# Performance work log

Hardware: AMD Instinct MI355X
Metric: run time of the kernel (lower is better)

## Reference

```python
import jax, jax.numpy as jnp
import numpy as np

N, T, D, H = 16, 1024, 1024, 1024


def setup_inputs() -> dict:
    key = jax.random.key(0)
    ks = jax.random.split(key, 7)
    x = jax.random.normal(ks[0], (N, T, D), dtype=jnp.float32)
    reset = jax.random.randint(ks[1], (N, T), 0, 2).astype(bool)
    carry = jax.random.normal(ks[2], (N, T, H), dtype=jnp.float32)
    # learned parameters (orthogonal-ish init approximated by scaled gaussian)
    initial_h = jax.random.normal(ks[3], (H,), dtype=jnp.float32) * 0.1
    w_i = jax.random.normal(ks[4], (D, 3 * H), dtype=jnp.float32) * (1.0 / np.sqrt(D))
    w_h = jax.random.normal(ks[5], (H, 3 * H), dtype=jnp.float32) * (1.0 / np.sqrt(H))
    b = jnp.zeros((3 * H,), dtype=jnp.float32)
    return {"x": x, "reset": reset, "carry": carry,
            "initial_h": initial_h, "w_i": w_i, "w_h": w_h, "b": b}


def _gru_scan(x, reset, carry, initial_h, w_i, w_h, b):
    n, t, _ = x.shape
    h_dim = initial_h.shape[0]
    # learn_initial_h and not is_target: replace carry with learned init where reset
    init_b = jnp.broadcast_to(initial_h, (n, t, h_dim))
    carry = jnp.where(reset[..., None], init_b, carry)
    # precompute input projections for all timesteps (math-equivalent hoist)
    gx = jnp.einsum('ntd,dk->ntk', x, w_i)  # [N,T,3H]
    w_h_zr, w_h_a = w_h[:, :2 * h_dim], w_h[:, 2 * h_dim:]
    b_zr, b_a = b[:2 * h_dim], b[2 * h_dim:]

    def step(h, inp):
        gx_t, reset_t, carry_t = inp  # [N,3H], [N], [N,H]
        h = jnp.where(reset_t[:, None], carry_t, h)
        zr = jax.nn.sigmoid(gx_t[:, :2 * h_dim] + h @ w_h_zr + b_zr)
        z, r = zr[:, :h_dim], zr[:, h_dim:]
        a = jnp.tanh(gx_t[:, 2 * h_dim:] + (r * h) @ w_h_a + b_a)
        h_next = (1.0 - z) * h + z * a
        return h_next, h_next

    h0 = carry[:, 0, :]  # scan init is carry_seq[:1,:] per batch element
    _, hs = jax.lax.scan(step, h0, (gx.transpose(1, 0, 2), reset.T, carry.transpose(1, 0, 2)))
    states = hs.transpose(1, 0, 2)  # [N,T,H]
    return states


def reference(x, reset, carry, initial_h, w_i, w_h, b):
    states = _gru_scan(x, reset, carry, initial_h, w_i, w_h, b)
    # hk.GRU returns (next_state, next_state): outputs_seq == states_seq
    return states, states, initial_h[None, :]
```

## Files before the change

### kernel.cpp

```cpp
#include <hip/hip_runtime.h>

typedef __attribute__((ext_vector_type(8))) short s8v;
typedef __attribute__((ext_vector_type(4))) float f4v;
typedef __attribute__((ext_vector_type(4))) unsigned int u4v;
typedef unsigned long long u64;

__device__ __forceinline__ float bf2f(unsigned short u) {
    union { float f; unsigned int i; } v; v.i = ((unsigned int)u) << 16; return v.f;
}
__device__ __forceinline__ unsigned short f2bf(float f) {
    union { float f; unsigned int i; } v; v.f = f;
    unsigned int x = v.i;
    return (unsigned short)((x + 0x7fffu + ((x >> 16) & 1u)) >> 16);
}
__device__ __forceinline__ float ldf(const void* p, size_t i, int f32) {
    return f32 ? ((const float*)p)[i] : bf2f(((const unsigned short*)p)[i]);
}

__device__ __forceinline__ s8v ald16(u64* p) {
    union { s8v v; u64 u[2]; } r;
    r.u[0] = __hip_atomic_load(p,     __ATOMIC_RELAXED, __HIP_MEMORY_SCOPE_AGENT);
    r.u[1] = __hip_atomic_load(p + 1, __ATOMIC_RELAXED, __HIP_MEMORY_SCOPE_AGENT);
    return r.v;
}
__device__ __forceinline__ void pack_store64p(u64* p, int lane, unsigned short val,
                                              bool do_store) {
    unsigned int mv = val;
    unsigned int lo = mv | (__shfl_down(mv, 16, 64) << 16);
    unsigned int hi = __shfl_down(mv, 32, 64) | (__shfl_down(mv, 48, 64) << 16);
    if (lane < 16 && do_store) {
        u64 q = (u64)lo | ((u64)hi << 32);
        __hip_atomic_store(p, q, __ATOMIC_RELAXED, __HIP_MEMORY_SCOPE_AGENT);
    }
}
__device__ __forceinline__ void pack_store64(u64* p, int lane, unsigned short val) {
    pack_store64p(p, lane, val, true);
}

__device__ __forceinline__ void pollwait(int* f, int v) {
    while (__hip_atomic_load(f, __ATOMIC_RELAXED, __HIP_MEMORY_SCOPE_AGENT) < v)
        __builtin_amdgcn_s_sleep(1);
    __builtin_amdgcn_sched_barrier(0);
    asm volatile("" ::: "memory");
}

__global__ void detect_k(const unsigned short* __restrict__ xu,
                         const unsigned int* __restrict__ rw,
                         int* __restrict__ flags) {
    __shared__ int cnt;
    int tid = threadIdx.x;
    if (tid == 0) cnt = 0;
    for (int i = tid + 8; i < 1040; i += 256) flags[i] = 0;
    __syncthreads();
    int bad = 0;
    for (int i = tid; i < 4096; i += 256) {
        unsigned short v = xu[i];
        int e = (v >> 7) & 0xFF;
        if (e == 0xFF || (e <= 90 && (v & 0x7FFFu) != 0)) bad++;
    }
    atomicAdd(&cnt, bad);
    __syncthreads();
    if (tid == 0) {
        flags[0] = (cnt > 16) ? 1 : 0;
        bool w01 = true, oddz = true, ones = false, b01 = true, h16 = true, fv = true;
        for (int i = 0; i < 32; ++i) {
            unsigned int w = rw[i];
            if (w > 1u) w01 = false;
            if ((i & 1) && w != 0u) oddz = false;
            if (w != 0u) ones = true;
            if ((w & 0xFFu) > 1u || ((w >> 8) & 0xFFu) > 1u ||
                ((w >> 16) & 0xFFu) > 1u || (w >> 24) > 1u) b01 = false;
            unsigned int lo = w & 0xFFFFu, hi = w >> 16;
            if (!((lo == 0u || lo == 0x3F80u) && (hi == 0u || hi == 0x3F80u))) h16 = false;
            if (!(w == 0u || w == 0x3F800000u)) fv = false;
        }
        int mode;
        if (w01 && oddz && ones) mode = 4;
        else if (w01) mode = 0;
        else if (fv) mode = 3;
        else if (h16) mode = 2;
        else if (b01) mode = 1;
        else mode = 0;
        flags[1] = mode;
    }
}

__device__ __forceinline__ int get_reset(const void* p, int mode, int idx) {
    switch (mode) {
        case 0: return ((const int*)p)[idx] != 0;
        case 1: return ((const signed char*)p)[idx] != 0;
        case 2: return ((const unsigned short*)p)[idx] != 0;
        case 3: return ((const float*)p)[idx] != 0.f;
        default: return ((const int*)p)[idx * 2] != 0;
    }
}

__device__ __forceinline__ void stage_w(const void* w, int wf32, int j0, int tid,
                                        unsigned short* lws) {
    for (int k = tid; k < 1024; k += 256) {
        #pragma unroll
        for (int g = 0; g < 3; ++g) {
            unsigned short tmp[8];
            size_t base = (size_t)k * 3072 + g * 1024 + j0;
            if (wf32) {
                const float* wf = (const float*)w;
                f4v v0 = *(const f4v*)&wf[base];
                f4v v1 = *(const f4v*)&wf[base + 4];
                #pragma unroll
                for (int r = 0; r < 4; ++r) { tmp[r] = f2bf(v0[r]); tmp[4 + r] = f2bf(v1[r]); }
            } else {
                union { u4v v; unsigned short u[8]; } cv;
                cv.v = *(const u4v*)&((const unsigned short*)w)[base];
                #pragma unroll
                for (int r = 0; r < 8; ++r) tmp[r] = cv.u[r];
            }
            #pragma unroll
            for (int r = 0; r < 8; ++r) lws[(g * 8 + r) * 1048 + k] = tmp[r];
        }
    }
}

__global__ __launch_bounds__(256, 1) void scan2g_k(
    const void* __restrict__ xv, const void* __restrict__ resetv,
    const void* __restrict__ carryv, const void* __restrict__ inithv,
    const void* __restrict__ wiv, const void* __restrict__ whv,
    const void* __restrict__ biasv, void* __restrict__ outv,
    unsigned short* __restrict__ hbuf0, unsigned short* __restrict__ hbuf1,
    unsigned short* __restrict__ rbuf0, unsigned short* __restrict__ rbuf1,
    int* __restrict__ flags) {
    __shared__ __align__(16) unsigned short lws[24 * 1048];
    float* lpA = (float*)lws;
    float* lpB = (float*)lws + 2048;
    float* lhe = (float*)lws + 4096;

    const int xf32 = flags[0];
    const int rmode = flags[1];
    int* fA[2] = { flags + 16,  flags + 272 };
    int* fB[2] = { flags + 528, flags + 784 };

    const int tid = threadIdx.x;
    const int wave = tid >> 6, lane = tid & 63;
    const int c = lane & 15, q = lane >> 4;
    const bool c8 = (c < 8);
    const int j0 = blockIdx.x * 8;
    const int an = tid & 15, ac = tid >> 4;
    const int jloc = ac & 7, jg = j0 + jloc;
    const bool owner = (ac < 8);
    const int colA = owner ? jg : (1024 + jg);
    const int colB = 2048 + jg;
    const float biasA = ldf(biasv, colA, xf32);
    const float biasB = ldf(biasv, colB, xf32);
    const float initj = ldf(inithv, jg, xf32);
    const unsigned short initj_b = f2bf(initj);
    const int kbase = wave * 256;
    const int qidx = an * 256 + (j0 >> 2) + (wave & 1);

    s8v zero8;
    { union { s8v v; u64 u[2]; } z; z.u[0] = 0; z.u[1] = 0; zero8 = z.v; }

    s8v whA[8], whB[8], wiA[8], wiB[8];
    stage_w(whv, xf32, j0, tid, lws);
    __syncthreads();
    #pragma unroll
    for (int kc = 0; kc < 8; ++kc) {
        int kk = kbase + kc * 32 + q * 8;
        whA[kc] = *(const s8v*)&lws[c * 1048 + kk];
        whB[kc] = *(const s8v*)&lws[(16 + (c & 7)) * 1048 + kk];
    }
    __syncthreads();
    stage_w(wiv, xf32, j0, tid, lws);
    __syncthreads();
    #pragma unroll
    for (int kc = 0; kc < 8; ++kc) {
        int kk = kbase + kc * 32 + q * 8;
        wiA[kc] = *(const s8v*)&lws[c * 1048 + kk];
        wiB[kc] = *(const s8v*)&lws[(16 + (c & 7)) * 1048 + kk];
    }
    __syncthreads();

    s8v xa0[8], xa1[8];
    #pragma unroll
    for (int kc = 0; kc < 8; ++kc) { xa0[kc] = zero8; xa1[kc] = zero8; }
    auto load_x2 = [&](int tt) {
        if (!c8) return;
        #pragma unroll
        for (int g = 0; g < 2; ++g) {
            s8v* xg = g ? xa1 : xa0;
            size_t row = (size_t)(g * 8 + c) * 1048576 + (size_t)tt * 1024;
            if (xf32) {
                const float* xf = (const float*)xv;
                #pragma unroll
                for (int kc = 0; kc < 8; ++kc) {
                    size_t b = row + kbase + kc * 32 + q * 8;
                    f4v v0 = *(const f4v*)&xf[b];
                    f4v v1 = *(const f4v*)&xf[b + 4];
                    union { s8v v; unsigned short u[8]; } cv;
                    #pragma unroll
                    for (int r = 0; r < 4; ++r) { cv.u[r] = f2bf(v0[r]); cv.u[4 + r] = f2bf(v1[r]); }
                    xg[kc] = cv.v;
                }
            } else {
                const unsigned short* xu = (const unsigned short*)xv;
                #pragma unroll
                for (int kc = 0; kc < 8; ++kc)
                    xg[kc] = *(const s8v*)&xu[row + kbase + kc * 32 + q * 8];
            }
        }
    };

    float hreg = 0.f, zreg = 0.f, he_own = 0.f;
    int rs_cur = 0;
    if (owner) {
        rs_cur = get_reset(resetv, rmode, an * 1024);
        float h0 = rs_cur ? initj : ldf(carryv, (size_t)an * 1048576 + jg, xf32);
        unsigned short hb0 = f2bf(h0);
        hreg = bf2f(hb0);
        pack_store64((u64*)hbuf0 + qidx, lane, hb0);
        if (an == 0) {
            if (xf32) ((float*)outv)[(size_t)33554432 + jg] = initj;
            else ((unsigned short*)outv)[(size_t)33554432 + jg] = initj_b;
        }
        asm volatile("s_waitcnt vmcnt(0)" ::: "memory");
        if (lane == 0) {
            __hip_atomic_store(&fB[0][blockIdx.x * 2 + wave], 1,
                               __ATOMIC_RELAXED, __HIP_MEMORY_SCOPE_AGENT);
            __hip_atomic_store(&fB[1][blockIdx.x * 2 + wave], 1,
                               __ATOMIC_RELAXED, __HIP_MEMORY_SCOPE_AGENT);
        }
    }
    load_x2(0);

    for (int t = 0; t < 1024; ++t) {
        unsigned short* hcur = (t & 1) ? hbuf1 : hbuf0;
        unsigned short* hnxt = (t & 1) ? hbuf0 : hbuf1;
        unsigned short* rcur = (t & 1) ? rbuf1 : rbuf0;

        int rs_next = 0;
        if (owner) {
            he_own = rs_cur ? initj : hreg;
            lhe[an * 8 + jloc] = he_own;
            if (t < 1023) rs_next = get_reset(resetv, rmode, an * 1024 + t + 1);
        }

        #pragma unroll
        for (int g = 0; g < 2; ++g) {
            pollwait(&fB[g][tid], t + 1);
            s8v ha[8];
            #pragma unroll
            for (int kc = 0; kc < 8; ++kc)
                ha[kc] = c8 ? ald16((u64*)hcur +
                          (((g * 8 + c) * 1024 + kbase + kc * 32 + q * 8) >> 2)) : zero8;
            f4v acc = (f4v){0.f, 0.f, 0.f, 0.f};
            #pragma unroll
            for (int kc = 0; kc < 8; ++kc)
                acc = __builtin_amdgcn_mfma_f32_16x16x32_bf16(ha[kc], whA[kc], acc, 0, 0, 0);
            const s8v* xg = g ? xa1 : xa0;
            #pragma unroll
            for (int kc = 0; kc < 8; ++kc)
                acc = __builtin_amdgcn_mfma_f32_16x16x32_bf16(xg[kc], wiA[kc], acc, 0, 0, 0);
            *(f4v*)&lpA[g * 1024 + wave * 256 + c * 16 + q * 4] = acc;
            __syncthreads();
            {
                int m = an & 7;
                float pre = lpA[g * 1024 + ac * 16 + m] + lpA[g * 1024 + 256 + ac * 16 + m] +
                            lpA[g * 1024 + 512 + ac * 16 + m] + lpA[g * 1024 + 768 + ac * 16 + m] + biasA;
                float sg = 1.f / (1.f + expf(-pre));
                bool gok = ((an >> 3) == g);
                if (owner) { if (gok) zreg = sg; }
                else {
                    pack_store64p((u64*)rcur + qidx, lane,
                                  f2bf(sg * lhe[an * 8 + jloc]), gok);
                    asm volatile("s_waitcnt vmcnt(0)" ::: "memory");
                    if (lane == 0)
                        __hip_atomic_store(&fA[g][blockIdx.x * 2 + (wave - 2)], t + 1,
                                           __ATOMIC_RELAXED, __HIP_MEMORY_SCOPE_AGENT);
                }
            }
        }

        #pragma unroll
        for (int g = 0; g < 2; ++g) {
            pollwait(&fA[g][tid], t + 1);
            s8v ra[8];
            #pragma unroll
            for (int kc = 0; kc < 8; ++kc)
                ra[kc] = c8 ? ald16((u64*)rcur +
                          (((g * 8 + c) * 1024 + kbase + kc * 32 + q * 8) >> 2)) : zero8;
            f4v acc2 = (f4v){0.f, 0.f, 0.f, 0.f};
            #pragma unroll
            for (int kc = 0; kc < 8; ++kc)
                acc2 = __builtin_amdgcn_mfma_f32_16x16x32_bf16(ra[kc], whB[kc], acc2, 0, 0, 0);
            const s8v* xg = g ? xa1 : xa0;
            #pragma unroll
            for (int kc = 0; kc < 8; ++kc)
                acc2 = __builtin_amdgcn_mfma_f32_16x16x32_bf16(xg[kc], wiB[kc], acc2, 0, 0, 0);
            *(f4v*)&lpB[g * 1024 + wave * 256 + c * 16 + q * 4] = acc2;
            __syncthreads();
            if (owner) {
                bool gok = ((an >> 3) == g);
                int m = an & 7;
                float preB = lpB[g * 1024 + ac * 16 + m] + lpB[g * 1024 + 256 + ac * 16 + m] +
                             lpB[g * 1024 + 512 + ac * 16 + m] + lpB[g * 1024 + 768 + ac * 16 + m] + biasB;
                float aa = tanhf(preB);
                float hn = (1.f - zreg) * he_own + zreg * aa;
                unsigned short hb = f2bf(hn);
                if (gok) hreg = hn;
                pack_store64p((u64*)hnxt + qidx, lane,
                              rs_next ? initj_b : hb, gok);
                asm volatile("s_waitcnt vmcnt(0)" ::: "memory");
                if (lane == 0)
                    __hip_atomic_store(&fB[g][blockIdx.x * 2 + wave], t + 2,
                                       __ATOMIC_RELAXED, __HIP_MEMORY_SCOPE_AGENT);
                if (gok) {
                    size_t oidx = ((size_t)an * 1024 + t) * 1024 + jg;
                    if (xf32) {
                        float* o = (float*)outv;
                        o[oidx] = hn;
                        o[16777216 + oidx] = hn;
                    } else {
                        unsigned short* o = (unsigned short*)outv;
                        o[oidx] = hb;
                        o[16777216 + oidx] = hb;
                    }
                }
            }
        }
        if (owner) rs_cur = rs_next;
        if (t < 1023) load_x2(t + 1);
    }

    if (blockIdx.x == 0) {
        pollwait(&fB[0][tid], 1025);
        pollwait(&fB[1][tid], 1025);
        __syncthreads();
        if (tid == 0)
            __hip_atomic_store(&flags[8], 1,
                               __ATOMIC_RELAXED, __HIP_MEMORY_SCOPE_AGENT);
    }
}

__global__ __launch_bounds__(256) void scan_fb(
    const void* __restrict__ xv, const void* __restrict__ resetv,
    const void* __restrict__ carryv, const void* __restrict__ inithv,
    const void* __restrict__ wiv, const void* __restrict__ whv,
    const void* __restrict__ biasv, void* __restrict__ outv,
    unsigned short* __restrict__ hbuf0, unsigned short* __restrict__ hbuf1,
    unsigned short* __restrict__ rbuf0, unsigned short* __restrict__ rbuf1,
    int* __restrict__ flags) {
    if (__hip_atomic_load(&flags[8], __ATOMIC_RELAXED,
                          __HIP_MEMORY_SCOPE_AGENT) != 0) return;

    __shared__ __align__(16) unsigned short lws[24 * 1048];
    __shared__ __align__(16) float lpartA[4 * 256];
    __shared__ __align__(16) float lpartB[4 * 256];
    __shared__ float lhe[128];

    const int xf32 = flags[0];
    const int rmode = flags[1];
    int* flagA = flags + 16;
    int* flagB = flags + 272;

    const int tid = threadIdx.x;
    const int wave = tid >> 6, lane = tid & 63;
    const int c = lane & 15, q = lane >> 4;
    const int j0 = blockIdx.x * 8;
    const int an = tid & 15, ac = tid >> 4;
    const int jloc = ac & 7, jg = j0 + jloc;
    const bool owner = (ac < 8);
    const int colA = owner ? jg : (1024 + jg);
    const int colB = 2048 + jg;
    const float biasA = ldf(biasv, colA, xf32);
    const float biasB = ldf(biasv, colB, xf32);
    const float initj = ldf(inithv, jg, xf32);
    const unsigned short initj_b = f2bf(initj);
    const int kbase = wave * 256;
    const int qidx = an * 256 + (j0 >> 2) + (wave & 1);

    s8v whA[8], whB[8], wiA[8], wiB[8];
    stage_w(whv, xf32, j0, tid, lws);
    __syncthreads();
    #pragma unroll
    for (int kc = 0; kc < 8; ++kc) {
        int kk = kbase + kc * 32 + q * 8;
        whA[kc] = *(const s8v*)&lws[c * 1048 + kk];
        whB[kc] = *(const s8v*)&lws[(16 + (c & 7)) * 1048 + kk];
    }
    __syncthreads();
    stage_w(wiv, xf32, j0, tid, lws);
    __syncthreads();
    #pragma unroll
    for (int kc = 0; kc < 8; ++kc) {
        int kk = kbase + kc * 32 + q * 8;
        wiA[kc] = *(const s8v*)&lws[c * 1048 + kk];
        wiB[kc] = *(const s8v*)&lws[(16 + (c & 7)) * 1048 + kk];
    }

    s8v xa[8];
    auto load_xa = [&](int tt) {
        if (xf32) {
            const float* xf = (const float*)xv;
            #pragma unroll
            for (int kc = 0; kc < 8; ++kc) {
                size_t b = (size_t)c * 1048576 + (size_t)tt * 1024 + kbase + kc * 32 + q * 8;
                f4v v0 = *(const f4v*)&xf[b];
                f4v v1 = *(const f4v*)&xf[b + 4];
                union { s8v v; unsigned short u[8]; } cv;
                #pragma unroll
                for (int r = 0; r < 4; ++r) { cv.u[r] = f2bf(v0[r]); cv.u[4 + r] = f2bf(v1[r]); }
                xa[kc] = cv.v;
            }
        } else {
            const unsigned short* xu = (const unsigned short*)xv;
            #pragma unroll
            for (int kc = 0; kc < 8; ++kc) {
                size_t b = (size_t)c * 1048576 + (size_t)tt * 1024 + kbase + kc * 32 + q * 8;
                xa[kc] = *(const s8v*)&xu[b];
            }
        }
    };

    float hreg = 0.f, zreg = 0.f, he_own = 0.f;
    int rs_cur = 0;
    if (owner) {
        rs_cur = get_reset(resetv, rmode, an * 1024);
        float h0 = rs_cur ? initj : ldf(carryv, (size_t)an * 1048576 + jg, xf32);
        unsigned short hb0 = f2bf(h0);
        hreg = bf2f(hb0);
        pack_store64((u64*)hbuf0 + qidx, lane, hb0);
        if (an == 0) {
            if (xf32) ((float*)outv)[(size_t)33554432 + jg] = initj;
            else ((unsigned short*)outv)[(size_t)33554432 + jg] = initj_b;
        }
        asm volatile("s_waitcnt vmcnt(0)" ::: "memory");
        if (lane == 0)
            __hip_atomic_store(&flagB[blockIdx.x * 2 + wave], 1,
                               __ATOMIC_RELAXED, __HIP_MEMORY_SCOPE_AGENT);
    }
    load_xa(0);

    for (int t = 0; t < 1024; ++t) {
        unsigned short* hcur = (t & 1) ? hbuf1 : hbuf0;
        unsigned short* hnxt = (t & 1) ? hbuf0 : hbuf1;
        unsigned short* rcur = (t & 1) ? rbuf1 : rbuf0;

        int rs_next = 0;
        if (owner) {
            he_own = rs_cur ? initj : hreg;
            lhe[an * 8 + jloc] = he_own;
            if (t < 1023) rs_next = get_reset(resetv, rmode, an * 1024 + t + 1);
        }

        f4v acc = (f4v){0.f, 0.f, 0.f, 0.f};
        #pragma unroll
        for (int kc = 0; kc < 8; ++kc)
            acc = __builtin_amdgcn_mfma_f32_16x16x32_bf16(xa[kc], wiA[kc], acc, 0, 0, 0);

        pollwait(&flagB[tid], t + 1);
        s8v ha[8];
        #pragma unroll
        for (int kc = 0; kc < 8; ++kc)
            ha[kc] = ald16((u64*)hcur + ((c * 1024 + kbase + kc * 32 + q * 8) >> 2));
        #pragma unroll
        for (int kc = 0; kc < 8; ++kc)
            acc = __builtin_amdgcn_mfma_f32_16x16x32_bf16(ha[kc], whA[kc], acc, 0, 0, 0);
        *(f4v*)&lpartA[wave * 256 + c * 16 + q * 4] = acc;
        __syncthreads();
        {
            float pre = lpartA[ac * 16 + an] + lpartA[256 + ac * 16 + an] +
                        lpartA[512 + ac * 16 + an] + lpartA[768 + ac * 16 + an] + biasA;
            float sg = 1.f / (1.f + expf(-pre));
            if (owner) zreg = sg;
            else {
                pack_store64((u64*)rcur + qidx, lane, f2bf(sg * lhe[an * 8 + jloc]));
                asm volatile("s_waitcnt vmcnt(0)" ::: "memory");
                if (lane == 0)
                    __hip_atomic_store(&flagA[blockIdx.x * 2 + (wave - 2)], t + 1,
                                       __ATOMIC_RELAXED, __HIP_MEMORY_SCOPE_AGENT);
            }
        }

        f4v acc2 = (f4v){0.f, 0.f, 0.f, 0.f};
        #pragma unroll
        for (int kc = 0; kc < 8; ++kc)
            acc2 = __builtin_amdgcn_mfma_f32_16x16x32_bf16(xa[kc], wiB[kc], acc2, 0, 0, 0);

        pollwait(&flagA[tid], t + 1);
        s8v ra[8];
        #pragma unroll
        for (int kc = 0; kc < 8; ++kc)
            ra[kc] = ald16((u64*)rcur + ((c * 1024 + kbase + kc * 32 + q * 8) >> 2));
        #pragma unroll
        for (int kc = 0; kc < 8; ++kc)
            acc2 = __builtin_amdgcn_mfma_f32_16x16x32_bf16(ra[kc], whB[kc], acc2, 0, 0, 0);
        *(f4v*)&lpartB[wave * 256 + c * 16 + q * 4] = acc2;
        __syncthreads();
        if (owner) {
            float preB = lpartB[ac * 16 + an] + lpartB[256 + ac * 16 + an] +
                         lpartB[512 + ac * 16 + an] + lpartB[768 + ac * 16 + an] + biasB;
            float aa = tanhf(preB);
            float hn = (1.f - zreg) * he_own + zreg * aa;
            unsigned short hb = f2bf(hn);
            hreg = hn;
            pack_store64((u64*)hnxt + qidx, lane, rs_next ? initj_b : hb);
            asm volatile("s_waitcnt vmcnt(0)" ::: "memory");
            if (lane == 0)
                __hip_atomic_store(&flagB[blockIdx.x * 2 + wave], t + 2,
                                   __ATOMIC_RELAXED, __HIP_MEMORY_SCOPE_AGENT);
            size_t oidx = ((size_t)an * 1024 + t) * 1024 + jg;
            if (xf32) {
                float* o = (float*)outv;
                o[oidx] = hn;
                o[16777216 + oidx] = hn;
            } else {
                unsigned short* o = (unsigned short*)outv;
                o[oidx] = hb;
                o[16777216 + oidx] = hb;
            }
            rs_cur = rs_next;
        }
        if (t < 1023) load_xa(t + 1);
    }
}

extern "C" void kernel_launch(void* const* d_in, const int* in_sizes, int n_in,
                              void* d_out, int out_size, void* d_ws, size_t ws_size,
                              hipStream_t stream) {
    const void* x     = d_in[0];
    const void* reset = d_in[1];
    const void* carry = d_in[2];
    const void* inith = d_in[3];
    const void* w_i   = d_in[4];
    const void* w_h   = d_in[5];
    const void* bias  = d_in[6];

    char* ws = (char*)d_ws;
    unsigned short* hbuf0 = (unsigned short*)ws;
    unsigned short* hbuf1 = (unsigned short*)(ws + 32768);
    unsigned short* rbuf0 = (unsigned short*)(ws + 65536);
    unsigned short* rbuf1 = (unsigned short*)(ws + 98304);
    int*            flags = (int*)(ws + 131072);

    detect_k<<<dim3(1), dim3(256), 0, stream>>>(
        (const unsigned short*)x, (const unsigned int*)reset, flags);

    void* kargs[] = { (void*)&x, (void*)&reset, (void*)&carry, (void*)&inith,
                      (void*)&w_i, (void*)&w_h, (void*)&bias, (void*)&d_out,
                      (void*)&hbuf0, (void*)&hbuf1, (void*)&rbuf0, (void*)&rbuf1,
                      (void*)&flags };

    hipError_t e2g = hipLaunchCooperativeKernel(
        reinterpret_cast<const void*>(&scan2g_k),
        dim3(128), dim3(256), kargs, 0, stream);
    (void)e2g;

    hipError_t efb = hipLaunchCooperativeKernel(
        reinterpret_cast<const void*>(&scan_fb),
        dim3(128), dim3(256), kargs, 0, stream);
    (void)efb;

    (void)in_sizes; (void)n_in; (void)out_size; (void)ws_size;
}
```

Baseline: 17.51 ms.

## Replace flag-based cross-block sync with per-element tagged h/r values

Replaces the separate ready-flag arrays and double-buffered h/r buffers with single buffers in which each 32-bit word packs a bf16 value with a timestep tag. Consumers poll the data words directly until the tags reach the current step, which removes the flag stores, the vmcnt waits before them and the separate flag polls. It also drops the two-group (8+8 batch) split and processes all 16 batch rows in one MFMA pass per gate, halving the number of block barriers per step. In exchange, each h/r load doubles in width, polling is spread over many words, and tag overflow or ordering assumptions must hold.

```diff
diff --git a/kernel.cpp b/kernel.cpp
--- a/kernel.cpp
+++ b/kernel.cpp
@@ -17,26 +17,26 @@
     return f32 ? ((const float*)p)[i] : bf2f(((const unsigned short*)p)[i]);
 }
 
+__device__ __forceinline__ u64 ald(u64* p) {
+    return __hip_atomic_load(p, __ATOMIC_RELAXED, __HIP_MEMORY_SCOPE_AGENT);
+}
 __device__ __forceinline__ s8v ald16(u64* p) {
     union { s8v v; u64 u[2]; } r;
-    r.u[0] = __hip_atomic_load(p,     __ATOMIC_RELAXED, __HIP_MEMORY_SCOPE_AGENT);
-    r.u[1] = __hip_atomic_load(p + 1, __ATOMIC_RELAXED, __HIP_MEMORY_SCOPE_AGENT);
+    r.u[0] = ald(p); r.u[1] = ald(p + 1);
     return r.v;
 }
-__device__ __forceinline__ void pack_store64p(u64* p, int lane, unsigned short val,
-                                              bool do_store) {
+__device__ __forceinline__ void ast32(unsigned int* p, unsigned int v) {
+    __hip_atomic_store(p, v, __ATOMIC_RELAXED, __HIP_MEMORY_SCOPE_AGENT);
+}
+__device__ __forceinline__ void pack_store64(u64* p, int lane, unsigned short val) {
     unsigned int mv = val;
     unsigned int lo = mv | (__shfl_down(mv, 16, 64) << 16);
     unsigned int hi = __shfl_down(mv, 32, 64) | (__shfl_down(mv, 48, 64) << 16);
-    if (lane < 16 && do_store) {
+    if (lane < 16) {
         u64 q = (u64)lo | ((u64)hi << 32);
         __hip_atomic_store(p, q, __ATOMIC_RELAXED, __HIP_MEMORY_SCOPE_AGENT);
     }
 }
-__device__ __forceinline__ void pack_store64(u64* p, int lane, unsigned short val) {
-    pack_store64p(p, lane, val, true);
-}
-
 __device__ __forceinline__ void pollwait(int* f, int v) {
     while (__hip_atomic_load(f, __ATOMIC_RELAXED, __HIP_MEMORY_SCOPE_AGENT) < v)
         __builtin_amdgcn_s_sleep(1);
@@ -46,11 +46,12 @@
 
 __global__ void detect_k(const unsigned short* __restrict__ xu,
                          const unsigned int* __restrict__ rw,
-                         int* __restrict__ flags) {
+                         int* __restrict__ flags, unsigned int* __restrict__ tags) {
     __shared__ int cnt;
     int tid = threadIdx.x;
     if (tid == 0) cnt = 0;
-    for (int i = tid + 8; i < 1040; i += 256) flags[i] = 0;
+    for (int i = tid; i < 32768; i += 256) tags[i] = 0;
+    for (int i = tid + 8; i < 528; i += 256) flags[i] = 0;
     __syncthreads();
     int bad = 0;
     for (int i = tid; i < 4096; i += 256) {
@@ -120,28 +121,29 @@
     }
 }
 
-__global__ __launch_bounds__(256, 1) void scan2g_k(
+__global__ __launch_bounds__(256, 1) void scan_tag_k(
     const void* __restrict__ xv, const void* __restrict__ resetv,
     const void* __restrict__ carryv, const void* __restrict__ inithv,
     const void* __restrict__ wiv, const void* __restrict__ whv,
     const void* __restrict__ biasv, void* __restrict__ outv,
-    unsigned short* __restrict__ hbuf0, unsigned short* __restrict__ hbuf1,
-    unsigned short* __restrict__ rbuf0, unsigned short* __restrict__ rbuf1,
+    unsigned short* __restrict__ hb0_, unsigned short* __restrict__ hb1_,
+    unsigned short* __restrict__ rb0_, unsigned short* __restrict__ rb1_,
     int* __restrict__ flags) {
+    unsigned int* htag = (unsigned int*)hb0_;
+    unsigned int* rtag = (unsigned int*)rb0_;
+    (void)hb1_; (void)rb1_;
+
     __shared__ __align__(16) unsigned short lws[24 * 1048];
-    float* lpA = (float*)lws;
-    float* lpB = (float*)lws + 2048;
-    float* lhe = (float*)lws + 4096;
+    __shared__ __align__(16) float lpartA[4 * 256];
+    __shared__ __align__(16) float lpartB[4 * 256];
+    __shared__ float lhe[128];
 
     const int xf32 = flags[0];
     const int rmode = flags[1];
-    int* fA[2] = { flags + 16,  flags + 272 };
-    int* fB[2] = { flags + 528, flags + 784 };
 
     const int tid = threadIdx.x;
     const int wave = tid >> 6, lane = tid & 63;
     const int c = lane & 15, q = lane >> 4;
-    const bool c8 = (c < 8);
     const int j0 = blockIdx.x * 8;
     const int an = tid & 15, ac = tid >> 4;
     const int jloc = ac & 7, jg = j0 + jloc;
@@ -153,10 +155,7 @@
     const float initj = ldf(inithv, jg, xf32);
     const unsigned short initj_b = f2bf(initj);
     const int kbase = wave * 256;
-    const int qidx = an * 256 + (j0 >> 2) + (wave & 1);
-
-    s8v zero8;
-    { union { s8v v; u64 u[2]; } z; z.u[0] = 0; z.u[1] = 0; zero8 = z.v; }
+    const int widx = an * 1024 + jg;
 
     s8v whA[8], whB[8], wiA[8], wiB[8];
     stage_w(whv, xf32, j0, tid, lws);
@@ -176,34 +175,66 @@
         wiA[kc] = *(const s8v*)&lws[c * 1048 + kk];
         wiB[kc] = *(const s8v*)&lws[(16 + (c & 7)) * 1048 + kk];
     }
-    __syncthreads();
-
-    s8v xa0[8], xa1[8];
-    #pragma unroll
-    for (int kc = 0; kc < 8; ++kc) { xa0[kc] = zero8; xa1[kc] = zero8; }
-    auto load_x2 = [&](int tt) {
-        if (!c8) return;
-        #pragma unroll
-        for (int g = 0; g < 2; ++g) {
-            s8v* xg = g ? xa1 : xa0;
-            size_t row = (size_t)(g * 8 + c) * 1048576 + (size_t)tt * 1024;
-            if (xf32) {
-                const float* xf = (const float*)xv;
+
+    auto read_half = [&](unsigned int* buf, int kc0, unsigned wtag, s8v* frag) {
+        u64 hv[16];
+        #pragma unroll
+        for (int kc = 0; kc < 4; ++kc) {
+            u64* p = (u64*)&buf[c * 1024 + kbase + (kc0 + kc) * 32 + q * 8];
+            #pragma unroll
+            for (int i = 0; i < 4; ++i) hv[kc * 4 + i] = ald(p + i);
+        }
+        bool ok;
+        do {
+            ok = true;
+            #pragma unroll
+            for (int kc = 0; kc < 4; ++kc) {
+                u64* p = (u64*)&buf[c * 1024 + kbase + (kc0 + kc) * 32 + q * 8];
                 #pragma unroll
-                for (int kc = 0; kc < 8; ++kc) {
-                    size_t b = row + kbase + kc * 32 + q * 8;
-                    f4v v0 = *(const f4v*)&xf[b];
-                    f4v v1 = *(const f4v*)&xf[b + 4];
-                    union { s8v v; unsigned short u[8]; } cv;
-                    #pragma unroll
-                    for (int r = 0; r < 4; ++r) { cv.u[r] = f2bf(v0[r]); cv.u[4 + r] = f2bf(v1[r]); }
-                    xg[kc] = cv.v;
+                for (int i = 0; i < 4; ++i) {
+                    u64 v = hv[kc * 4 + i];
+                    if (((unsigned)(v >> 16) & 0xFFFFu) < wtag ||
+                        (unsigned)(v >> 48) < wtag) {
+                        hv[kc * 4 + i] = ald(p + i);
+                        ok = false;
+                    }
                 }
-            } else {
-                const unsigned short* xu = (const unsigned short*)xv;
+            }
+            if (!ok) __builtin_amdgcn_s_sleep(1);
+        } while (!ok);
+        #pragma unroll
+        for (int kc = 0; kc < 4; ++kc) {
+            union { s8v v; unsigned short u[8]; } cv;
+            #pragma unroll
+            for (int i = 0; i < 4; ++i) {
+                u64 v = hv[kc * 4 + i];
+                cv.u[2 * i]     = (unsigned short)(v & 0xFFFFu);
+                cv.u[2 * i + 1] = (unsigned short)((v >> 32) & 0xFFFFu);
+            }
+            frag[kc] = cv.v;
+        }
+    };
+
+    s8v xa[8];
+    auto load_xa = [&](int tt) {
+        if (xf32) {
+            const float* xf = (const float*)xv;
+            #pragma unroll
+            for (int kc = 0; kc < 8; ++kc) {
+                size_t b = (size_t)c * 1048576 + (size_t)tt * 1024 + kbase + kc * 32 + q * 8;
+                f4v v0 = *(const f4v*)&xf[b];
+                f4v v1 = *(const f4v*)&xf[b + 4];
+                union { s8v v; unsigned short u[8]; } cv;
                 #pragma unroll
-                for (int kc = 0; kc < 8; ++kc)
-                    xg[kc] = *(const s8v*)&xu[row + kbase + kc * 32 + q * 8];
+                for (int r = 0; r < 4; ++r) { cv.u[r] = f2bf(v0[r]); cv.u[4 + r] = f2bf(v1[r]); }
+                xa[kc] = cv.v;
+            }
+        } else {
+            const unsigned short* xu = (const unsigned short*)xv;
+            #pragma unroll
+            for (int kc = 0; kc < 8; ++kc) {
+                size_t b = (size_t)c * 1048576 + (size_t)tt * 1024 + kbase + kc * 32 + q * 8;
+                xa[kc] = *(const s8v*)&xu[b];
             }
         }
     };
@@ -215,25 +246,16 @@
         float h0 = rs_cur ? initj : ldf(carryv, (size_t)an * 1048576 + jg, xf32);
         unsigned short hb0 = f2bf(h0);
         hreg = bf2f(hb0);
-        pack_store64((u64*)hbuf0 + qidx, lane, hb0);
+        ast32(&htag[widx], (1u << 16) | hb0);
         if (an == 0) {
             if (xf32) ((float*)outv)[(size_t)33554432 + jg] = initj;
             else ((unsigned short*)outv)[(size_t)33554432 + jg] = initj_b;
         }
-        asm volatile("s_waitcnt vmcnt(0)" ::: "memory");
-        if (lane == 0) {
-            __hip_atomic_store(&fB[0][blockIdx.x * 2 + wave], 1,
-                               __ATOMIC_RELAXED, __HIP_MEMORY_SCOPE_AGENT);
-            __hip_atomic_store(&fB[1][blockIdx.x * 2 + wave], 1,
-                               __ATOMIC_RELAXED, __HIP_MEMORY_SCOPE_AGENT);
-        }
-    }
-    load_x2(0);
+    }
+    load_xa(0);
 
     for (int t = 0; t < 1024; ++t) {
-        unsigned short* hcur = (t & 1) ? hbuf1 : hbuf0;
-        unsigned short* hnxt = (t & 1) ? hbuf0 : hbuf1;
-        unsigned short* rcur = (t & 1) ? rbuf1 : rbuf0;
+        const unsigned wtag = (unsigned)(t + 1);
 
         int rs_next = 0;
         if (owner) {
@@ -242,96 +264,77 @@
             if (t < 1023) rs_next = get_reset(resetv, rmode, an * 1024 + t + 1);
         }
 
-        #pragma unroll
-        for (int g = 0; g < 2; ++g) {
-            pollwait(&fB[g][tid], t + 1);
-            s8v ha[8];
-            #pragma unroll
-            for (int kc = 0; kc < 8; ++kc)
-                ha[kc] = c8 ? ald16((u64*)hcur +
-                          (((g * 8 + c) * 1024 + kbase + kc * 32 + q * 8) >> 2)) : zero8;
-            f4v acc = (f4v){0.f, 0.f, 0.f, 0.f};
-            #pragma unroll
-            for (int kc = 0; kc < 8; ++kc)
+        f4v acc = (f4v){0.f, 0.f, 0.f, 0.f};
+        #pragma unroll
+        for (int kc = 0; kc < 8; ++kc)
+            acc = __builtin_amdgcn_mfma_f32_16x16x32_bf16(xa[kc], wiA[kc], acc, 0, 0, 0);
+        {
+            s8v ha[4];
+            read_half(htag, 0, wtag, ha);
+            #pragma unroll
+            for (int kc = 0; kc < 4; ++kc)
                 acc = __builtin_amdgcn_mfma_f32_16x16x32_bf16(ha[kc], whA[kc], acc, 0, 0, 0);
-            const s8v* xg = g ? xa1 : xa0;
-            #pragma unroll
-            for (int kc = 0; kc < 8; ++kc)
-                acc = __builtin_amdgcn_mfma_f32_16x16x32_bf16(xg[kc], wiA[kc], acc, 0, 0, 0);
-            *(f4v*)&lpA[g * 1024 + wave * 256 + c * 16 + q * 4] = acc;
-            __syncthreads();
-            {
-                int m = an & 7;
-                float pre = lpA[g * 1024 + ac * 16 + m] + lpA[g * 1024 + 256 + ac * 16 + m] +
-                            lpA[g * 1024 + 512 + ac * 16 + m] + lpA[g * 1024 + 768 + ac * 16 + m] + biasA;
-                float sg = 1.f / (1.f + expf(-pre));
-                bool gok = ((an >> 3) == g);
-                if (owner) { if (gok) zreg = sg; }
-                else {
-                    pack_store64p((u64*)rcur + qidx, lane,
-                                  f2bf(sg * lhe[an * 8 + jloc]), gok);
-                    asm volatile("s_waitcnt vmcnt(0)" ::: "memory");
-                    if (lane == 0)
-                        __hip_atomic_store(&fA[g][blockIdx.x * 2 + (wave - 2)], t + 1,
-                                           __ATOMIC_RELAXED, __HIP_MEMORY_SCOPE_AGENT);
-                }
-            }
-        }
-
-        #pragma unroll
-        for (int g = 0; g < 2; ++g) {
-            pollwait(&fA[g][tid], t + 1);
-            s8v ra[8];
-            #pragma unroll
-            for (int kc = 0; kc < 8; ++kc)
-                ra[kc] = c8 ? ald16((u64*)rcur +
-                          (((g * 8 + c) * 1024 + kbase + kc * 32 + q * 8) >> 2)) : zero8;
-            f4v acc2 = (f4v){0.f, 0.f, 0.f, 0.f};
-            #pragma unroll
-            for (int kc = 0; kc < 8; ++kc)
+            read_half(htag, 4, wtag, ha);
+            #pragma unroll
+            for (int kc = 0; kc < 4; ++kc)
+                acc = __builtin_amdgcn_mfma_f32_16x16x32_bf16(ha[kc], whA[4 + kc], acc, 0, 0, 0);
+        }
+        *(f4v*)&lpartA[wave * 256 + c * 16 + q * 4] = acc;
+        __syncthreads();
+        {
+            float pre = lpartA[ac * 16 + an] + lpartA[256 + ac * 16 + an] +
+                        lpartA[512 + ac * 16 + an] + lpartA[768 + ac * 16 + an] + biasA;
+            float sg = 1.f / (1.f + expf(-pre));
+            if (owner) zreg = sg;
+            else ast32(&rtag[widx], (wtag << 16) | f2bf(sg * lhe[an * 8 + jloc]));
+        }
+
+        f4v acc2 = (f4v){0.f, 0.f, 0.f, 0.f};
+        #pragma unroll
+        for (int kc = 0; kc < 8; ++kc)
+            acc2 = __builtin_amdgcn_mfma_f32_16x16x32_bf16(xa[kc], wiB[kc], acc2, 0, 0, 0);
+        {
+            s8v ra[4];
+            read_half(rtag, 0, wtag, ra);
+            #pragma unroll
+            for (int kc = 0; kc < 4; ++kc)
                 acc2 = __builtin_amdgcn_mfma_f32_16x16x32_bf16(ra[kc], whB[kc], acc2, 0, 0, 0);
-            const s8v* xg = g ? xa1 : xa0;
-            #pragma unroll
-            for (int kc = 0; kc < 8; ++kc)
-                acc2 = __builtin_amdgcn_mfma_f32_16x16x32_bf16(xg[kc], wiB[kc], acc2, 0, 0, 0);
-            *(f4v*)&lpB[g * 1024 + wave * 256 + c * 16 + q * 4] = acc2;
-            __syncthreads();
-            if (owner) {
-                bool gok = ((an >> 3) == g);
-                int m = an & 7;
-                float preB = lpB[g * 1024 + ac * 16 + m] + lpB[g * 1024 + 256 + ac * 16 + m] +
-                             lpB[g * 1024 + 512 + ac * 16 + m] + lpB[g * 1024 + 768 + ac * 16 + m] + biasB;
-                float aa = tanhf(preB);
-                float hn = (1.f - zreg) * he_own + zreg * aa;
-                unsigned short hb = f2bf(hn);
-                if (gok) hreg = hn;
-                pack_store64p((u64*)hnxt + qidx, lane,
-                              rs_next ? initj_b : hb, gok);
-                asm volatile("s_waitcnt vmcnt(0)" ::: "memory");
-                if (lane == 0)
-                    __hip_atomic_store(&fB[g][blockIdx.x * 2 + wave], t + 2,
-                                       __ATOMIC_RELAXED, __HIP_MEMORY_SCOPE_AGENT);
-                if (gok) {
-                    size_t oidx = ((size_t)an * 1024 + t) * 1024 + jg;
-                    if (xf32) {
-                        float* o = (float*)outv;
-                        o[oidx] = hn;
-                        o[16777216 + oidx] = hn;
-                    } else {
-                        unsigned short* o = (unsigned short*)outv;
-                        o[oidx] = hb;
-                        o[16777216 + oidx] = hb;
-                    }
-                }
-            }
-        }
-        if (owner) rs_cur = rs_next;
-        if (t < 1023) load_x2(t + 1);
+            read_half(rtag, 4, wtag, ra);
+            #pragma unroll
+            for (int kc = 0; kc < 4; ++kc)
+                acc2 = __builtin_amdgcn_mfma_f32_16x16x32_bf16(ra[kc], whB[4 + kc], acc2, 0, 0, 0);
+        }
+        *(f4v*)&lpartB[wave * 256 + c * 16 + q * 4] = acc2;
+        __syncthreads();
+        if (owner) {
+            float preB = lpartB[ac * 16 + an] + lpartB[256 + ac * 16 + an] +
+                         lpartB[512 + ac * 16 + an] + lpartB[768 + ac * 16 + an] + biasB;
+            float aa = tanhf(preB);
+            float hn = (1.f - zreg) * he_own + zreg * aa;
+            unsigned short hb = f2bf(hn);
+            hreg = hn;
+            ast32(&htag[widx], ((wtag + 1) << 16) | (unsigned)(rs_next ? initj_b : hb));
+            size_t oidx = ((size_t)an * 1024 + t) * 1024 + jg;
+            if (xf32) {
+                float* o = (float*)outv;
+                o[oidx] = hn;
+                o[16777216 + oidx] = hn;
+            } else {
+                unsigned short* o = (unsigned short*)outv;
+                o[oidx] = hb;
+                o[16777216 + oidx] = hb;
+            }
+            rs_cur = rs_next;
+        }
+        if (t < 1023) load_xa(t + 1);
     }
 
     if (blockIdx.x == 0) {
-        pollwait(&fB[0][tid], 1025);
-        pollwait(&fB[1][tid], 1025);
+        for (int i = tid; i < 16384; i += 256) {
+            while ((__hip_atomic_load(&htag[i], __ATOMIC_RELAXED,
+                                      __HIP_MEMORY_SCOPE_AGENT) >> 16) < 1025u)
+                __builtin_amdgcn_s_sleep(1);
+        }
         __syncthreads();
         if (tid == 0)
             __hip_atomic_store(&flags[8], 1,
@@ -541,17 +544,18 @@
     int*            flags = (int*)(ws + 131072);
 
     detect_k<<<dim3(1), dim3(256), 0, stream>>>(
-        (const unsigned short*)x, (const unsigned int*)reset, flags);
+        (const unsigned short*)x, (const unsigned int*)reset, flags,
+        (unsigned int*)ws);
 
     void* kargs[] = { (void*)&x, (void*)&reset, (void*)&carry, (void*)&inith,
                       (void*)&w_i, (void*)&w_h, (void*)&bias, (void*)&d_out,
                       (void*)&hbuf0, (void*)&hbuf1, (void*)&rbuf0, (void*)&rbuf1,
                       (void*)&flags };
 
-    hipError_t e2g = hipLaunchCooperativeKernel(
-        reinterpret_cast<const void*>(&scan2g_k),
+    hipError_t etg = hipLaunchCooperativeKernel(
+        reinterpret_cast<const void*>(&scan_tag_k),
         dim3(128), dim3(256), kargs, 0, stream);
-    (void)e2g;
+    (void)etg;
 
     hipError_t efb = hipLaunchCooperativeKernel(
         reinterpret_cast<const void*>(&scan_fb),
```

After: 16.20 ms. 7.5% less time.
